# Kernel optimization log

Hardware: AMD Instinct MI355X
Metric: run time of the kernel (lower is better)

## Reference

```python
import jax, jax.numpy as jnp
import numpy as np

B, D, N, C = 256, 2048, 65536, 8192  # batch, feat dim, memory-bank size, num clusters
TEMP = 0.05


def setup_inputs() -> dict:
    key = jax.random.key(0)
    k1, k2, k3, k4 = jax.random.split(key, 4)
    inputs = jax.random.normal(k1, (B, D), jnp.float32)
    inputs = inputs / jnp.linalg.norm(inputs, axis=1, keepdims=True)
    features = jax.random.normal(k2, (N, D), jnp.float32)
    features = features / jnp.linalg.norm(features, axis=1, keepdims=True)
    labels = jax.random.randint(k3, (N,), 0, C).astype(jnp.int64)
    labels = labels.at[0].set(C - 1)  # pin labels.max()+1 == C (torch uses data-dependent size)
    indexes = jax.random.randint(k4, (B,), 0, N).astype(jnp.int64)
    return {"inputs": inputs, "indexes": indexes, "features": features, "labels": labels}


def reference(inputs, indexes, features, labels):
    # HM.forward: similarity of batch against full memory bank (momentum update is a
    # backward-pass buffer side effect, not part of the differentiable graph)
    sims = inputs @ features.T                                   # [B, N]
    targets = labels[indexes]                                    # [B]
    # per-sample soft cluster centers over same-label memory entries
    attn_mask = (targets[:, None] == labels[None, :]).astype(sims.dtype)  # [B, N]
    centers = (attn_mask * sims) @ features                      # [B, D]
    diag = jnp.einsum('bd,bd->b', inputs, centers) / TEMP        # diag of inputs_raw @ centers.T / temp
    logits = sims / TEMP                                         # [B, N]
    # cluster-averaged similarities: index_add over labels == segment_sum
    sim = jax.ops.segment_sum(logits.T, labels, num_segments=C)  # [C, B]
    nums = jax.ops.segment_sum(jnp.ones((N,), logits.dtype), labels, num_segments=C)  # [C]
    cmask = (nums > 0).astype(logits.dtype)                      # [C]
    sim = sim / jnp.where(nums > 0, nums, 1.0)[:, None]
    # replace each sample's own-cluster entry with its center similarity
    cols = jnp.arange(B)
    onehot = jnp.zeros((C, B), logits.dtype).at[targets, cols].set(1.0)
    score = jnp.zeros((C, B), logits.dtype).at[targets, cols].set(diag)
    sim = sim * (1.0 - onehot) + score                           # [C, B]
    # masked softmax over clusters (unstabilized exp, faithful to original)
    exps = jnp.exp(sim.T) * cmask[None, :]                       # [B, C]
    masked_sim = exps / (exps.sum(axis=1, keepdims=True) + 1e-6)
    logp = jnp.log(masked_sim + 1e-6)
    return -jnp.mean(logp[cols, targets])                        # nll_loss, mean reduction
```

## Files before the change

### kernel.cpp

```cpp
#include <hip/hip_runtime.h>

#define BATCH 256
#define DIM   2048
#define NMEM  65536
#define NCLUS 8192
#define TEMP  0.05f

typedef __attribute__((ext_vector_type(8))) short bf16x8;
typedef __attribute__((ext_vector_type(4))) float f32x4;
typedef __attribute__((ext_vector_type(4))) unsigned short u16x4;
typedef __attribute__((ext_vector_type(8))) unsigned short u16x8;

__device__ inline unsigned short f2bf(float f) {
    unsigned u = __float_as_uint(f);
    u += 0x7fffu + ((u >> 16) & 1u);
    return (unsigned short)(u >> 16);
}

__global__ void k_init(const int* __restrict__ labels, const int* __restrict__ indexes,
                       int* __restrict__ nums, int* __restrict__ targets) {
    int gid = blockIdx.x * 256 + threadIdx.x;
    if (gid < NMEM) atomicAdd(&nums[labels[gid]], 1);
    if (gid < BATCH) targets[gid] = labels[indexes[gid]];
}

__global__ void k_scan(const int* __restrict__ nums, int* __restrict__ offs) {
    __shared__ int part[256];
    int t = threadIdx.x;
    int base = t * 32;
    int local[32];
    int s = 0;
    #pragma unroll
    for (int i = 0; i < 32; i++) { local[i] = s; s += nums[base + i]; }
    part[t] = s;
    __syncthreads();
    for (int d = 1; d < 256; d <<= 1) {
        int v = (t >= d) ? part[t - d] : 0;
        __syncthreads();
        part[t] += v;
        __syncthreads();
    }
    int cb = (t == 0) ? 0 : part[t - 1];
    #pragma unroll
    for (int i = 0; i < 32; i++) offs[base + i] = cb + local[i];
}

__global__ void k_scatter(const int* __restrict__ labels, const int* __restrict__ offs,
                          int* __restrict__ cursor, int* __restrict__ order) {
    int n = blockIdx.x * 256 + threadIdx.x;
    int c = labels[n];
    int pos = atomicAdd(&cursor[c], 1);
    order[offs[c] + pos] = n;
}

__global__ void k_convA(const float* __restrict__ inputs, unsigned short* __restrict__ A_sw) {
    int gid = blockIdx.x * 256 + threadIdx.x;
    int e = gid * 8;
    int r = e >> 11;
    int k = e & 2047;
    const float4* p = (const float4*)(inputs + (size_t)r * DIM + k);
    float4 f0 = p[0], f1 = p[1];
    u16x8 o;
    o[0] = f2bf(f0.x); o[1] = f2bf(f0.y); o[2] = f2bf(f0.z); o[3] = f2bf(f0.w);
    o[4] = f2bf(f1.x); o[5] = f2bf(f1.y); o[6] = f2bf(f1.z); o[7] = f2bf(f1.w);
    *(u16x8*)(A_sw + (size_t)(k >> 5) * (BATCH * 32) + r * 32 + (k & 31)) = o;
}

__global__ __launch_bounds__(256) void k_agg(const float* __restrict__ feats,
                                             const int* __restrict__ order,
                                             const int* __restrict__ offs,
                                             const int* __restrict__ nums,
                                             unsigned short* __restrict__ csum) {
    int c = blockIdx.x;
    int t = threadIdx.x;
    int cnt = nums[c], off = offs[c];
    float acc[8] = {0.f, 0.f, 0.f, 0.f, 0.f, 0.f, 0.f, 0.f};
    int nn = (cnt > 0) ? order[off] : 0;
    for (int i = 0; i < cnt; i++) {
        int ncur = nn;
        if (i + 1 < cnt) nn = order[off + i + 1];
        const float4* p = (const float4*)(feats + (size_t)ncur * DIM + t * 8);
        float4 a = p[0], b = p[1];
        acc[0] += a.x; acc[1] += a.y; acc[2] += a.z; acc[3] += a.w;
        acc[4] += b.x; acc[5] += b.y; acc[6] += b.z; acc[7] += b.w;
    }
    u16x8 o;
    #pragma unroll
    for (int j = 0; j < 8; j++) o[j] = f2bf(acc[j]);
    *(u16x8*)(csum + (size_t)c * DIM + t * 8) = o;
}

__global__ __launch_bounds__(256) void k_gemm2(const unsigned short* __restrict__ csum,
                                               const unsigned short* __restrict__ A_sw,
                                               float* __restrict__ simP) {
    __shared__ short As[BATCH * 32];
    __shared__ short Bs[64 * 32];
    int tid = threadIdx.x;
    int w = tid >> 6, l = tid & 63;
    int n0 = blockIdx.x * 64;
    int kc = blockIdx.y;
    int ar = l & 15, aq = l >> 4;

    f32x4 acc[4][4];
    #pragma unroll
    for (int i = 0; i < 4; i++)
        #pragma unroll
        for (int j = 0; j < 4; j++) acc[i][j] = (f32x4){0.f, 0.f, 0.f, 0.f};

    const char* bgbase = (const char*)(csum + (size_t)(n0 + (tid >> 2)) * DIM + (tid & 3) * 8);

    for (int ss = 0; ss < 16; ss++) {
        int s = kc * 16 + ss;
        __syncthreads();
        {
            const char* gbase = (const char*)A_sw + (size_t)s * 16384;
            #pragma unroll
            for (int i = 0; i < 4; i++) {
                int ofs = ((w << 2) + i) * 1024;
                __builtin_amdgcn_global_load_lds(
                    (const __attribute__((address_space(1))) void*)(gbase + ofs + l * 16),
                    (__attribute__((address_space(3))) void*)((char*)As + ofs),
                    16, 0, 0);
            }
        }
        {
            __builtin_amdgcn_global_load_lds(
                (const __attribute__((address_space(1))) void*)(bgbase + (size_t)s * 64),
                (__attribute__((address_space(3))) void*)((char*)Bs + w * 1024),
                16, 0, 0);
        }
        __syncthreads();
        bf16x8 a[4], b[4];
        #pragma unroll
        for (int i = 0; i < 4; i++) a[i] = *(const bf16x8*)&As[(w * 64 + i * 16 + ar) * 32 + aq * 8];
        #pragma unroll
        for (int j = 0; j < 4; j++) b[j] = *(const bf16x8*)&Bs[(j * 16 + ar) * 32 + aq * 8];
        #pragma unroll
        for (int i = 0; i < 4; i++)
            #pragma unroll
            for (int j = 0; j < 4; j++)
                acc[i][j] = __builtin_amdgcn_mfma_f32_16x16x32_bf16(a[i], b[j], acc[i][j], 0, 0, 0);
    }
    float* outp = simP + (size_t)kc * (NCLUS * BATCH);
    #pragma unroll
    for (int i = 0; i < 4; i++) {
        int row = w * 64 + i * 16 + aq * 4;
        #pragma unroll
        for (int j = 0; j < 4; j++) {
            int col = n0 + j * 16 + ar;
            *(f32x4*)&outp[(size_t)col * BATCH + row] = acc[i][j];
        }
    }
}

__global__ void k_diag(const float* __restrict__ inputs, const float* __restrict__ feats,
                       const int* __restrict__ order, const int* __restrict__ offs,
                       const int* __restrict__ nums, const int* __restrict__ targets,
                       float* __restrict__ numval) {
    int b = blockIdx.x, t = threadIdx.x;
    int c = targets[b];
    int cnt = nums[c], off = offs[c];
    const float4* ip = (const float4*)(inputs + (size_t)b * DIM + t * 8);
    float4 x0 = ip[0], x1 = ip[1];
    __shared__ float red[256];
    float d2 = 0.f;
    for (int i = 0; i < cnt; i++) {
        int n = order[off + i];
        const float4* fp = (const float4*)(feats + (size_t)n * DIM + t * 8);
        float4 a = fp[0], bb = fp[1];
        float part = x0.x * a.x + x0.y * a.y + x0.z * a.z + x0.w * a.w
                   + x1.x * bb.x + x1.y * bb.y + x1.z * bb.z + x1.w * bb.w;
        red[t] = part;
        __syncthreads();
        for (int d = 128; d > 0; d >>= 1) {
            if (t < d) red[t] += red[t + d];
            __syncthreads();
        }
        if (t == 0) { float dot = red[0]; d2 += dot * dot; }
        __syncthreads();
    }
    if (t == 0) numval[b] = __expf(d2 * (1.f / TEMP));
}

__global__ void k_reduce2(const float* __restrict__ simP, const int* __restrict__ nums,
                          const int* __restrict__ targets, const float* __restrict__ numval,
                          float* __restrict__ partial) {
    int p = blockIdx.x, t = threadIdx.x;
    int tgt = targets[t];
    float nv = numval[t];
    float tot = 0.f;
    const size_t CB = (size_t)NCLUS * BATCH;
    for (int j = 0; j < 128; j++) {
        int c = p * 128 + j;
        int cnt = nums[c];
        if (cnt == 0) continue;
        size_t a = (size_t)c * BATCH + t;
        float s = simP[a] + simP[CB + a] + simP[2 * CB + a] + simP[3 * CB + a];
        float val = (tgt == c) ? nv : __expf(s / ((float)cnt * TEMP));
        tot += val;
    }
    partial[p * 256 + t] = tot;
}

__global__ void k_loss(const float* __restrict__ partial, const float* __restrict__ numval,
                       float* __restrict__ out) {
    __shared__ float red[256];
    int t = threadIdx.x;
    float tot = 0.f;
    #pragma unroll
    for (int p = 0; p < 64; p++) tot += partial[p * 256 + t];
    float ls = -logf(numval[t] / (tot + 1e-6f) + 1e-6f);
    red[t] = ls;
    __syncthreads();
    for (int d = 128; d > 0; d >>= 1) {
        if (t < d) red[t] += red[t + d];
        __syncthreads();
    }
    if (t == 0) out[0] = red[0] / (float)BATCH;
}

extern "C" void kernel_launch(void* const* d_in, const int* in_sizes, int n_in,
                              void* d_out, int out_size, void* d_ws, size_t ws_size,
                              hipStream_t stream) {
    const float* inputs  = (const float*)d_in[0];
    const int*   indexes = (const int*)d_in[1];
    const float* feats   = (const float*)d_in[2];
    const int*   labels  = (const int*)d_in[3];
    float* out = (float*)d_out;

    char* ws = (char*)d_ws;
    size_t off = 0;
    unsigned short* csum = (unsigned short*)(ws + off); off += (size_t)NCLUS * DIM * 2;
    unsigned short* A_sw = (unsigned short*)(ws + off); off += (size_t)BATCH * DIM * 2;
    float* simP    = (float*)(ws + off); off += (size_t)4 * NCLUS * BATCH * 4;
    int*   nums    = (int*)(ws + off);   off += NCLUS * 4;
    int*   cursor  = (int*)(ws + off);   off += NCLUS * 4;
    int*   offs    = (int*)(ws + off);   off += NCLUS * 4;
    int*   order   = (int*)(ws + off);   off += (size_t)NMEM * 4;
    int*   targets = (int*)(ws + off);   off += BATCH * 4;
    float* partial = (float*)(ws + off); off += 64 * BATCH * 4;
    float* numval  = (float*)(ws + off); off += BATCH * 4;

    hipMemsetAsync(nums, 0, NCLUS * 4 + NCLUS * 4, stream);

    k_init   <<<NMEM / 256, 256, 0, stream>>>(labels, indexes, nums, targets);
    k_scan   <<<1, 256, 0, stream>>>(nums, offs);
    k_scatter<<<NMEM / 256, 256, 0, stream>>>(labels, offs, cursor, order);
    k_convA  <<<(BATCH * DIM / 8) / 256, 256, 0, stream>>>(inputs, A_sw);
    k_agg    <<<NCLUS, 256, 0, stream>>>(feats, order, offs, nums, csum);
    dim3 g2(NCLUS / 64, 4);
    k_gemm2  <<<g2, 256, 0, stream>>>(csum, A_sw, simP);
    k_diag   <<<BATCH, 256, 0, stream>>>(inputs, feats, order, offs, nums, targets, numval);
    k_reduce2<<<64, 256, 0, stream>>>(simP, nums, targets, numval, partial);
    k_loss   <<<1, 256, 0, stream>>>(partial, numval, out);
}
```

Baseline: 808.3 us.

## Fuse softmax denominator into double-buffered GEMM and merge conversion into init

Replaces the split-K GEMM, which wrote four partial similarity planes, with a single full-K GEMM over 32-cluster tiles. Its epilogue applies the exp and count scaling and accumulates per-sample denominators with atomics, so the reduce kernel and the large intermediate buffer go away. The GEMM gets double-buffered LDS, explicit vmcnt waits and XOR-swizzled A/B layouts. The bf16 conversion of the inputs is folded into the init kernel, k_diag uses per-wave shuffle reductions instead of block-wide barriers, and k_agg uses nontemporal loads. In exchange the GEMM has fewer blocks (256) with no split-K, and float atomics make the summation order nondeterministic.

```diff
diff --git a/kernel.cpp b/kernel.cpp
--- a/kernel.cpp
+++ b/kernel.cpp
@@ -8,8 +8,11 @@
 
 typedef __attribute__((ext_vector_type(8))) short bf16x8;
 typedef __attribute__((ext_vector_type(4))) float f32x4;
-typedef __attribute__((ext_vector_type(4))) unsigned short u16x4;
 typedef __attribute__((ext_vector_type(8))) unsigned short u16x8;
+
+#define GLDS(srcp, dstp) __builtin_amdgcn_global_load_lds( \
+    (const __attribute__((address_space(1))) void*)(srcp), \
+    (__attribute__((address_space(3))) void*)(dstp), 16, 0, 0)
 
 __device__ inline unsigned short f2bf(float f) {
     unsigned u = __float_as_uint(f);
@@ -18,43 +21,12 @@
 }
 
 __global__ void k_init(const int* __restrict__ labels, const int* __restrict__ indexes,
-                       int* __restrict__ nums, int* __restrict__ targets) {
+                       const float* __restrict__ inputs,
+                       int* __restrict__ nums, int* __restrict__ targets,
+                       unsigned short* __restrict__ A_sw) {
     int gid = blockIdx.x * 256 + threadIdx.x;
-    if (gid < NMEM) atomicAdd(&nums[labels[gid]], 1);
+    atomicAdd(&nums[labels[gid]], 1);
     if (gid < BATCH) targets[gid] = labels[indexes[gid]];
-}
-
-__global__ void k_scan(const int* __restrict__ nums, int* __restrict__ offs) {
-    __shared__ int part[256];
-    int t = threadIdx.x;
-    int base = t * 32;
-    int local[32];
-    int s = 0;
-    #pragma unroll
-    for (int i = 0; i < 32; i++) { local[i] = s; s += nums[base + i]; }
-    part[t] = s;
-    __syncthreads();
-    for (int d = 1; d < 256; d <<= 1) {
-        int v = (t >= d) ? part[t - d] : 0;
-        __syncthreads();
-        part[t] += v;
-        __syncthreads();
-    }
-    int cb = (t == 0) ? 0 : part[t - 1];
-    #pragma unroll
-    for (int i = 0; i < 32; i++) offs[base + i] = cb + local[i];
-}
-
-__global__ void k_scatter(const int* __restrict__ labels, const int* __restrict__ offs,
-                          int* __restrict__ cursor, int* __restrict__ order) {
-    int n = blockIdx.x * 256 + threadIdx.x;
-    int c = labels[n];
-    int pos = atomicAdd(&cursor[c], 1);
-    order[offs[c] + pos] = n;
-}
-
-__global__ void k_convA(const float* __restrict__ inputs, unsigned short* __restrict__ A_sw) {
-    int gid = blockIdx.x * 256 + threadIdx.x;
     int e = gid * 8;
     int r = e >> 11;
     int k = e & 2047;
@@ -63,7 +35,37 @@
     u16x8 o;
     o[0] = f2bf(f0.x); o[1] = f2bf(f0.y); o[2] = f2bf(f0.z); o[3] = f2bf(f0.w);
     o[4] = f2bf(f1.x); o[5] = f2bf(f1.y); o[6] = f2bf(f1.z); o[7] = f2bf(f1.w);
-    *(u16x8*)(A_sw + (size_t)(k >> 5) * (BATCH * 32) + r * 32 + (k & 31)) = o;
+    int slot = ((k >> 3) & 3) ^ (r & 3);
+    *(u16x8*)(A_sw + (size_t)(k >> 5) * (BATCH * 32) + r * 32 + slot * 8) = o;
+}
+
+__global__ void k_scan(const int* __restrict__ nums, int* __restrict__ offs) {
+    __shared__ int part[256];
+    int t = threadIdx.x;
+    int base = t * 32;
+    int local[32];
+    int s = 0;
+    #pragma unroll
+    for (int i = 0; i < 32; i++) { local[i] = s; s += nums[base + i]; }
+    part[t] = s;
+    __syncthreads();
+    for (int d = 1; d < 256; d <<= 1) {
+        int v = (t >= d) ? part[t - d] : 0;
+        __syncthreads();
+        part[t] += v;
+        __syncthreads();
+    }
+    int cb = (t == 0) ? 0 : part[t - 1];
+    #pragma unroll
+    for (int i = 0; i < 32; i++) offs[base + i] = cb + local[i];
+}
+
+__global__ void k_scatter(const int* __restrict__ labels, const int* __restrict__ offs,
+                          int* __restrict__ cursor, int* __restrict__ order) {
+    int n = blockIdx.x * 256 + threadIdx.x;
+    int c = labels[n];
+    int pos = atomicAdd(&cursor[c], 1);
+    order[offs[c] + pos] = n;
 }
 
 __global__ __launch_bounds__(256) void k_agg(const float* __restrict__ feats,
@@ -79,137 +81,161 @@
     for (int i = 0; i < cnt; i++) {
         int ncur = nn;
         if (i + 1 < cnt) nn = order[off + i + 1];
-        const float4* p = (const float4*)(feats + (size_t)ncur * DIM + t * 8);
-        float4 a = p[0], b = p[1];
-        acc[0] += a.x; acc[1] += a.y; acc[2] += a.z; acc[3] += a.w;
-        acc[4] += b.x; acc[5] += b.y; acc[6] += b.z; acc[7] += b.w;
+        const f32x4* p = (const f32x4*)(feats + (size_t)ncur * DIM + t * 8);
+        f32x4 a = __builtin_nontemporal_load(p);
+        f32x4 b = __builtin_nontemporal_load(p + 1);
+        acc[0] += a[0]; acc[1] += a[1]; acc[2] += a[2]; acc[3] += a[3];
+        acc[4] += b[0]; acc[5] += b[1]; acc[6] += b[2]; acc[7] += b[3];
     }
     u16x8 o;
     #pragma unroll
     for (int j = 0; j < 8; j++) o[j] = f2bf(acc[j]);
     *(u16x8*)(csum + (size_t)c * DIM + t * 8) = o;
-}
-
-__global__ __launch_bounds__(256) void k_gemm2(const unsigned short* __restrict__ csum,
-                                               const unsigned short* __restrict__ A_sw,
-                                               float* __restrict__ simP) {
-    __shared__ short As[BATCH * 32];
-    __shared__ short Bs[64 * 32];
-    int tid = threadIdx.x;
-    int w = tid >> 6, l = tid & 63;
-    int n0 = blockIdx.x * 64;
-    int kc = blockIdx.y;
-    int ar = l & 15, aq = l >> 4;
-
-    f32x4 acc[4][4];
-    #pragma unroll
-    for (int i = 0; i < 4; i++)
-        #pragma unroll
-        for (int j = 0; j < 4; j++) acc[i][j] = (f32x4){0.f, 0.f, 0.f, 0.f};
-
-    const char* bgbase = (const char*)(csum + (size_t)(n0 + (tid >> 2)) * DIM + (tid & 3) * 8);
-
-    for (int ss = 0; ss < 16; ss++) {
-        int s = kc * 16 + ss;
-        __syncthreads();
-        {
-            const char* gbase = (const char*)A_sw + (size_t)s * 16384;
-            #pragma unroll
-            for (int i = 0; i < 4; i++) {
-                int ofs = ((w << 2) + i) * 1024;
-                __builtin_amdgcn_global_load_lds(
-                    (const __attribute__((address_space(1))) void*)(gbase + ofs + l * 16),
-                    (__attribute__((address_space(3))) void*)((char*)As + ofs),
-                    16, 0, 0);
-            }
-        }
-        {
-            __builtin_amdgcn_global_load_lds(
-                (const __attribute__((address_space(1))) void*)(bgbase + (size_t)s * 64),
-                (__attribute__((address_space(3))) void*)((char*)Bs + w * 1024),
-                16, 0, 0);
-        }
-        __syncthreads();
-        bf16x8 a[4], b[4];
-        #pragma unroll
-        for (int i = 0; i < 4; i++) a[i] = *(const bf16x8*)&As[(w * 64 + i * 16 + ar) * 32 + aq * 8];
-        #pragma unroll
-        for (int j = 0; j < 4; j++) b[j] = *(const bf16x8*)&Bs[(j * 16 + ar) * 32 + aq * 8];
-        #pragma unroll
-        for (int i = 0; i < 4; i++)
-            #pragma unroll
-            for (int j = 0; j < 4; j++)
-                acc[i][j] = __builtin_amdgcn_mfma_f32_16x16x32_bf16(a[i], b[j], acc[i][j], 0, 0, 0);
-    }
-    float* outp = simP + (size_t)kc * (NCLUS * BATCH);
-    #pragma unroll
-    for (int i = 0; i < 4; i++) {
-        int row = w * 64 + i * 16 + aq * 4;
-        #pragma unroll
-        for (int j = 0; j < 4; j++) {
-            int col = n0 + j * 16 + ar;
-            *(f32x4*)&outp[(size_t)col * BATCH + row] = acc[i][j];
-        }
-    }
 }
 
 __global__ void k_diag(const float* __restrict__ inputs, const float* __restrict__ feats,
                        const int* __restrict__ order, const int* __restrict__ offs,
                        const int* __restrict__ nums, const int* __restrict__ targets,
                        float* __restrict__ numval) {
-    int b = blockIdx.x, t = threadIdx.x;
+    int b = blockIdx.x;
+    int tid = threadIdx.x;
+    int w = tid >> 6, l = tid & 63;
     int c = targets[b];
     int cnt = nums[c], off = offs[c];
-    const float4* ip = (const float4*)(inputs + (size_t)b * DIM + t * 8);
-    float4 x0 = ip[0], x1 = ip[1];
-    __shared__ float red[256];
+    const float4* ip = (const float4*)(inputs + (size_t)b * DIM);
+    float4 x[8];
+    #pragma unroll
+    for (int p = 0; p < 4; p++) {
+        x[2 * p]     = ip[p * 128 + l * 2];
+        x[2 * p + 1] = ip[p * 128 + l * 2 + 1];
+    }
     float d2 = 0.f;
-    for (int i = 0; i < cnt; i++) {
+    for (int i = w; i < cnt; i += 4) {
         int n = order[off + i];
-        const float4* fp = (const float4*)(feats + (size_t)n * DIM + t * 8);
-        float4 a = fp[0], bb = fp[1];
-        float part = x0.x * a.x + x0.y * a.y + x0.z * a.z + x0.w * a.w
-                   + x1.x * bb.x + x1.y * bb.y + x1.z * bb.z + x1.w * bb.w;
-        red[t] = part;
-        __syncthreads();
-        for (int d = 128; d > 0; d >>= 1) {
-            if (t < d) red[t] += red[t + d];
-            __syncthreads();
-        }
-        if (t == 0) { float dot = red[0]; d2 += dot * dot; }
-        __syncthreads();
-    }
-    if (t == 0) numval[b] = __expf(d2 * (1.f / TEMP));
-}
-
-__global__ void k_reduce2(const float* __restrict__ simP, const int* __restrict__ nums,
-                          const int* __restrict__ targets, const float* __restrict__ numval,
-                          float* __restrict__ partial) {
-    int p = blockIdx.x, t = threadIdx.x;
-    int tgt = targets[t];
-    float nv = numval[t];
-    float tot = 0.f;
-    const size_t CB = (size_t)NCLUS * BATCH;
-    for (int j = 0; j < 128; j++) {
-        int c = p * 128 + j;
-        int cnt = nums[c];
-        if (cnt == 0) continue;
-        size_t a = (size_t)c * BATCH + t;
-        float s = simP[a] + simP[CB + a] + simP[2 * CB + a] + simP[3 * CB + a];
-        float val = (tgt == c) ? nv : __expf(s / ((float)cnt * TEMP));
-        tot += val;
-    }
-    partial[p * 256 + t] = tot;
-}
-
-__global__ void k_loss(const float* __restrict__ partial, const float* __restrict__ numval,
+        const float4* fp = (const float4*)(feats + (size_t)n * DIM);
+        float dot = 0.f;
+        #pragma unroll
+        for (int p = 0; p < 4; p++) {
+            float4 f0 = fp[p * 128 + l * 2];
+            float4 f1 = fp[p * 128 + l * 2 + 1];
+            dot += x[2*p].x * f0.x + x[2*p].y * f0.y + x[2*p].z * f0.z + x[2*p].w * f0.w
+                 + x[2*p+1].x * f1.x + x[2*p+1].y * f1.y + x[2*p+1].z * f1.z + x[2*p+1].w * f1.w;
+        }
+        #pragma unroll
+        for (int m = 32; m >= 1; m >>= 1) dot += __shfl_xor(dot, m, 64);
+        d2 += dot * dot;
+    }
+    __shared__ float red[4];
+    if (l == 0) red[w] = d2;
+    __syncthreads();
+    if (tid == 0) numval[b] = __expf((red[0] + red[1] + red[2] + red[3]) * (1.f / TEMP));
+}
+
+__global__ __launch_bounds__(256) void k_gemm(const unsigned short* __restrict__ csum,
+                                              const unsigned short* __restrict__ A_sw,
+                                              const int* __restrict__ nums,
+                                              const int* __restrict__ targets,
+                                              float* __restrict__ denom) {
+    __shared__ short As[2][BATCH * 32];
+    __shared__ short Bs[2][32 * 64];
+    __shared__ int   s_tgt[BATCH];
+    int tid = threadIdx.x;
+    int w = tid >> 6, l = tid & 63;
+    int n0 = blockIdx.x * 32;
+    int ar = l & 15, aq = l >> 4;
+
+    s_tgt[tid] = targets[tid];
+
+    int br = w * 8 + (l >> 3);
+    int bg = (l & 7) ^ (l >> 3);
+    const char* bsrc = (const char*)(csum + (size_t)(n0 + br) * DIM + bg * 8);
+
+    {
+        const char* g = (const char*)A_sw;
+        #pragma unroll
+        for (int i = 0; i < 4; i++) {
+            int ofs = w * 4096 + i * 1024;
+            GLDS(g + ofs + l * 16, (char*)&As[0][0] + ofs);
+        }
+        GLDS(bsrc, (char*)&Bs[0][0] + w * 1024);
+    }
+
+    f32x4 acc[4][2];
+    #pragma unroll
+    for (int i = 0; i < 4; i++) {
+        acc[i][0] = (f32x4){0.f, 0.f, 0.f, 0.f};
+        acc[i][1] = (f32x4){0.f, 0.f, 0.f, 0.f};
+    }
+    __syncthreads();
+
+    for (int ks = 0; ks < 64; ks++) {
+        int cab = ks & 1;
+        int cbb = (ks >> 1) & 1;
+        if (ks + 1 < 64) {
+            const char* g = (const char*)A_sw + (size_t)(ks + 1) * 16384;
+            #pragma unroll
+            for (int i = 0; i < 4; i++) {
+                int ofs = w * 4096 + i * 1024;
+                GLDS(g + ofs + l * 16, (char*)&As[cab ^ 1][0] + ofs);
+            }
+        }
+        if (((ks & 1) == 0) && ks + 2 < 64) {
+            GLDS(bsrc + (size_t)(ks + 2) * 64, (char*)&Bs[cbb ^ 1][0] + w * 1024);
+        }
+        if (ks == 63)                        asm volatile("s_waitcnt vmcnt(0)" ::: "memory");
+        else if (((ks & 1) == 0) && ks < 62) asm volatile("s_waitcnt vmcnt(5)" ::: "memory");
+        else                                 asm volatile("s_waitcnt vmcnt(4)" ::: "memory");
+        __builtin_amdgcn_s_barrier();
+
+        const short* Ab = &As[cab][0];
+        const short* Bb = &Bs[cbb][0];
+        int gsb = (ks & 1) * 4;
+        bf16x8 a[4], b[2];
+        #pragma unroll
+        for (int i = 0; i < 4; i++)
+            a[i] = *(const bf16x8*)&Ab[(w * 64 + i * 16 + ar) * 32 + ((aq ^ (ar & 3)) * 8)];
+        #pragma unroll
+        for (int j = 0; j < 2; j++)
+            b[j] = *(const bf16x8*)&Bb[(j * 16 + ar) * 64 + (((gsb + aq) ^ (ar & 7)) * 8)];
+        #pragma unroll
+        for (int i = 0; i < 4; i++) {
+            acc[i][0] = __builtin_amdgcn_mfma_f32_16x16x32_bf16(a[i], b[0], acc[i][0], 0, 0, 0);
+            acc[i][1] = __builtin_amdgcn_mfma_f32_16x16x32_bf16(a[i], b[1], acc[i][1], 0, 0, 0);
+        }
+        __builtin_amdgcn_s_barrier();
+    }
+
+    int c0 = n0 + ar, c1 = n0 + 16 + ar;
+    int cnt0 = nums[c0], cnt1 = nums[c1];
+    float sc0 = (float)cnt0 * TEMP, sc1 = (float)cnt1 * TEMP;
+    float rs[16];
+    #pragma unroll
+    for (int i = 0; i < 4; i++) {
+        #pragma unroll
+        for (int r = 0; r < 4; r++) {
+            int bi = w * 64 + i * 16 + aq * 4 + r;
+            int tg = s_tgt[bi];
+            float v = 0.f;
+            if (cnt0 > 0 && tg != c0) v += __expf(acc[i][0][r] / sc0);
+            if (cnt1 > 0 && tg != c1) v += __expf(acc[i][1][r] / sc1);
+            #pragma unroll
+            for (int m = 1; m < 16; m <<= 1) v += __shfl_xor(v, m, 64);
+            rs[i * 4 + r] = v;
+        }
+    }
+    float myv = 0.f;
+    #pragma unroll
+    for (int t = 0; t < 16; t++) if (ar == t) myv = rs[t];
+    atomicAdd(&denom[w * 64 + (ar >> 2) * 16 + aq * 4 + (ar & 3)], myv);
+}
+
+__global__ void k_loss(const float* __restrict__ denom, const float* __restrict__ numval,
                        float* __restrict__ out) {
     __shared__ float red[256];
     int t = threadIdx.x;
-    float tot = 0.f;
-    #pragma unroll
-    for (int p = 0; p < 64; p++) tot += partial[p * 256 + t];
-    float ls = -logf(numval[t] / (tot + 1e-6f) + 1e-6f);
+    float nv = numval[t];
+    float tot = denom[t] + nv;
+    float ls = -logf(nv / (tot + 1e-6f) + 1e-6f);
     red[t] = ls;
     __syncthreads();
     for (int d = 128; d > 0; d >>= 1) {
@@ -232,25 +258,21 @@
     size_t off = 0;
     unsigned short* csum = (unsigned short*)(ws + off); off += (size_t)NCLUS * DIM * 2;
     unsigned short* A_sw = (unsigned short*)(ws + off); off += (size_t)BATCH * DIM * 2;
-    float* simP    = (float*)(ws + off); off += (size_t)4 * NCLUS * BATCH * 4;
     int*   nums    = (int*)(ws + off);   off += NCLUS * 4;
     int*   cursor  = (int*)(ws + off);   off += NCLUS * 4;
+    float* denom   = (float*)(ws + off); off += BATCH * 4;
     int*   offs    = (int*)(ws + off);   off += NCLUS * 4;
     int*   order   = (int*)(ws + off);   off += (size_t)NMEM * 4;
     int*   targets = (int*)(ws + off);   off += BATCH * 4;
-    float* partial = (float*)(ws + off); off += 64 * BATCH * 4;
     float* numval  = (float*)(ws + off); off += BATCH * 4;
 
-    hipMemsetAsync(nums, 0, NCLUS * 4 + NCLUS * 4, stream);
-
-    k_init   <<<NMEM / 256, 256, 0, stream>>>(labels, indexes, nums, targets);
+    hipMemsetAsync(nums, 0, NCLUS * 4 + NCLUS * 4 + BATCH * 4, stream);
+
+    k_init   <<<NMEM / 256, 256, 0, stream>>>(labels, indexes, inputs, nums, targets, A_sw);
     k_scan   <<<1, 256, 0, stream>>>(nums, offs);
     k_scatter<<<NMEM / 256, 256, 0, stream>>>(labels, offs, cursor, order);
-    k_convA  <<<(BATCH * DIM / 8) / 256, 256, 0, stream>>>(inputs, A_sw);
     k_agg    <<<NCLUS, 256, 0, stream>>>(feats, order, offs, nums, csum);
-    dim3 g2(NCLUS / 64, 4);
-    k_gemm2  <<<g2, 256, 0, stream>>>(csum, A_sw, simP);
     k_diag   <<<BATCH, 256, 0, stream>>>(inputs, feats, order, offs, nums, targets, numval);
-    k_reduce2<<<64, 256, 0, stream>>>(simP, nums, targets, numval, partial);
-    k_loss   <<<1, 256, 0, stream>>>(partial, numval, out);
-}
+    k_gemm   <<<NCLUS / 32, 256, 0, stream>>>(csum, A_sw, nums, targets, denom);
+    k_loss   <<<1, 256, 0, stream>>>(denom, numval, out);
+}
```

Result: faster. 762.6 us (-5.7%).
